# Optimization experiments

Measured on AMD Instinct MI355X. Metric: run time of the kernel, lower is better.

## Reference

```python
import jax, jax.numpy as jnp
import numpy as np

DIM = 384
RED = 16
PAIR = 128
EPS = 1e-5


def setup_inputs() -> dict:
    key = jax.random.key(0)
    ks = jax.random.split(key, 6)
    b, m = 2, 512
    x = jax.random.normal(ks[0], (b, m, DIM), dtype=jnp.float32)
    ln_gamma = jnp.ones((DIM,), dtype=jnp.float32)
    ln_beta = jnp.zeros((DIM,), dtype=jnp.float32)
    w_red = jax.random.normal(ks[1], (DIM, RED), dtype=jnp.float32) / np.sqrt(DIM)
    b_red = jax.random.normal(ks[2], (RED,), dtype=jnp.float32) * 0.02
    w_out = jax.random.normal(ks[3], (RED * RED, PAIR), dtype=jnp.float32) / np.sqrt(RED * RED)
    b_out = jax.random.normal(ks[4], (PAIR,), dtype=jnp.float32) * 0.02
    return {"x": x, "ln_gamma": ln_gamma, "ln_beta": ln_beta,
            "w_red": w_red, "b_red": b_red, "w_out": w_out, "b_out": b_out}


def reference(x, ln_gamma, ln_beta, w_red, b_red, w_out, b_out):
    # LayerNorm over last dim (eps=1e-5, torch default)
    mu = jnp.mean(x, axis=-1, keepdims=True)
    var = jnp.mean(jnp.square(x - mu), axis=-1, keepdims=True)
    xn = (x - mu) * jax.lax.rsqrt(var + EPS) * ln_gamma + ln_beta
    # Linear dim -> 16
    xr = jnp.einsum('bmd,dr->bmr', xn, w_red) + b_red  # (b, m, 16)
    # Full pairwise outer product + projection: same math as
    # einsum('bmi,bnj->bmnij') -> reshape (i j) -> Linear(256, pair_dim),
    # fused so the (i,j) axes contract directly with w_out reshaped to (16,16,pair).
    wr = w_out.reshape(RED, RED, PAIR)
    out = jnp.einsum('bmi,bnj,ijp->bmnp', xr, xr, wr) + b_out  # (b, m, m, pair)
    return out
```

## Files before the change

kernel.cpp:

```cpp
#include <hip/hip_runtime.h>
#include <hip/hip_bf16.h>

#define DIM 384
#define RED 16
#define PAIR 128
#define B 2
#define M 512
#define EPSV 1e-5f
#define LSTR 133

typedef float f32x4 __attribute__((ext_vector_type(4)));
typedef short bf16x8 __attribute__((ext_vector_type(8)));

__device__ __forceinline__ unsigned short f2bf(float f) {
  union { float f; unsigned u; } v; v.f = f;
  unsigned r = v.u + 0x7fffu + ((v.u >> 16) & 1u);
  return (unsigned short)(r >> 16);
}

__global__ __launch_bounds__(128) void opm_k1(
    const float* __restrict__ x, const float* __restrict__ g,
    const float* __restrict__ be, const float* __restrict__ w_red,
    const float* __restrict__ b_red, const float* __restrict__ w_out,
    unsigned short* __restrict__ xr_bf, unsigned short* __restrict__ T_bf) {
  const int row0 = blockIdx.x * 2;
  const int tid  = threadIdx.x;
  const int wave = tid >> 6;
  const int lane = tid & 63;

  __shared__ float xn_s[2][DIM];
  __shared__ float xr_s[2][RED];
  __shared__ float psum[2][4][RED];

  {
    const int row = row0 + wave;
    const float* xrow = x + (size_t)row * DIM;
    float v[6];
    #pragma unroll
    for (int k = 0; k < 6; ++k) v[k] = xrow[lane + 64 * k];
    float s = 0.f, sq = 0.f;
    #pragma unroll
    for (int k = 0; k < 6; ++k) { s += v[k]; sq += v[k] * v[k]; }
    #pragma unroll
    for (int off = 32; off > 0; off >>= 1) {
      s  += __shfl_xor(s, off);
      sq += __shfl_xor(sq, off);
    }
    const float mean = s * (1.0f / DIM);
    const float var  = sq * (1.0f / DIM) - mean * mean;
    const float rstd = rsqrtf(var + EPSV);
    #pragma unroll
    for (int k = 0; k < 6; ++k) {
      const int d = lane + 64 * k;
      xn_s[wave][d] = (v[k] - mean) * rstd * g[d] + be[d];
    }
  }
  __syncthreads();

  {
    const int rw = wave, r = lane & 15, part = lane >> 4;
    const int d0 = part * 96;
    float ps = 0.f;
    #pragma unroll 4
    for (int d = d0; d < d0 + 96; ++d) ps += xn_s[rw][d] * w_red[d * RED + r];
    psum[rw][part][r] = ps;
  }
  __syncthreads();
  if (tid < 32) {
    const int rw = tid >> 4, r = tid & 15;
    float v = b_red[r];
    #pragma unroll
    for (int qq = 0; qq < 4; ++qq) v += psum[rw][qq][r];
    xr_s[rw][r] = v;
    xr_bf[(size_t)(row0 + rw) * RED + r] = f2bf(v);
  }
  __syncthreads();

  {
    const int p = tid;
    const float* W = w_out + p;
    float a0[RED], a1[RED];
    #pragma unroll
    for (int i = 0; i < RED; ++i) {
      float s0 = 0.f, s1 = 0.f;
      #pragma unroll
      for (int j = 0; j < RED; ++j) {
        const float w = W[(i * RED + j) * PAIR];
        s0 += xr_s[0][j] * w;
        s1 += xr_s[1][j] * w;
      }
      a0[i] = s0; a1[i] = s1;
    }
    unsigned int* dst0 = (unsigned int*)(T_bf + ((size_t)row0 * PAIR + p) * RED);
    unsigned int* dst1 = (unsigned int*)(T_bf + ((size_t)(row0 + 1) * PAIR + p) * RED);
    #pragma unroll
    for (int k = 0; k < 8; ++k) {
      dst0[k] = (unsigned)f2bf(a0[2*k]) | ((unsigned)f2bf(a0[2*k+1]) << 16);
      dst1[k] = (unsigned)f2bf(a1[2*k]) | ((unsigned)f2bf(a1[2*k+1]) << 16);
    }
  }
}

__global__ __launch_bounds__(256) void opm_k2(
    const unsigned short* __restrict__ xr_bf, const unsigned short* __restrict__ T_bf,
    const float* __restrict__ b_out, float* __restrict__ out) {
  const int nb = blockIdx.x & 127;
  const int mt = (blockIdx.x >> 7) & 7;
  const int b  = blockIdx.x >> 10;
  const int tid  = threadIdx.x;
  const int wave = tid >> 6;
  const int lane = tid & 63;
  const int q = lane >> 4;
  const int r = lane & 15;
  const int n = nb * 4 + wave;

  __shared__ float lds[64 * LSTR];

  bf16x8 bv[8];
  const unsigned short* Tb = T_bf + ((size_t)(b * M + n) * PAIR) * RED;
  #pragma unroll
  for (int pb = 0; pb < 8; ++pb) {
    bf16x8 v = {0, 0, 0, 0, 0, 0, 0, 0};
    if (q < 2) v = *(const bf16x8*)(Tb + (pb * 16 + r) * RED + q * 8);
    bv[pb] = v;
  }
  float bias[8];
  #pragma unroll
  for (int pb = 0; pb < 8; ++pb) bias[pb] = b_out[pb * 16 + r];

  const int inner  = tid & 127;
  const int n_loc  = inner >> 5;
  const int p4     = (inner & 31) * 4;
  const int mlb    = tid >> 7;

  #pragma unroll
  for (int ms = 0; ms < 4; ++ms) {
    const int m0 = mt * 64 + ms * 16;
    bf16x8 av = {0, 0, 0, 0, 0, 0, 0, 0};
    if (q < 2) av = *(const bf16x8*)(xr_bf + (size_t)(b * M + m0 + r) * RED + q * 8);

    #pragma unroll
    for (int pb = 0; pb < 8; ++pb) {
      f32x4 acc = {bias[pb], bias[pb], bias[pb], bias[pb]};
      acc = __builtin_amdgcn_mfma_f32_16x16x32_bf16(av, bv[pb], acc, 0, 0, 0);
      float* dst = &lds[(wave * 16 + q * 4) * LSTR + pb * 16 + r];
      dst[0]        = acc[0];
      dst[LSTR]     = acc[1];
      dst[2 * LSTR] = acc[2];
      dst[3 * LSTR] = acc[3];
    }
    __syncthreads();

    float* ob = out + ((size_t)(b * M + m0 + mlb) * M + (nb * 4 + n_loc)) * PAIR + p4;
    #pragma unroll
    for (int ps = 0; ps < 8; ++ps) {
      const int m_loc = mlb + ps * 2;
      const f32x4 v = *(const f32x4*)&lds[(n_loc * 16 + m_loc) * LSTR + p4];
      *(f32x4*)(ob + (size_t)ps * 2 * M * PAIR) = v;
    }
    __syncthreads();
  }
}

extern "C" void kernel_launch(void* const* d_in, const int* in_sizes, int n_in,
                              void* d_out, int out_size, void* d_ws, size_t ws_size,
                              hipStream_t stream) {
  const float* x       = (const float*)d_in[0];
  const float* ln_g    = (const float*)d_in[1];
  const float* ln_b    = (const float*)d_in[2];
  const float* w_red   = (const float*)d_in[3];
  const float* b_red   = (const float*)d_in[4];
  const float* w_out   = (const float*)d_in[5];
  const float* b_out   = (const float*)d_in[6];
  float* out = (float*)d_out;

  unsigned short* xr_bf = (unsigned short*)d_ws;
  unsigned short* T_bf  = xr_bf + (size_t)B * M * RED;

  opm_k1<<<B * M / 2, 128, 0, stream>>>(x, ln_g, ln_b, w_red, b_red, w_out, xr_bf, T_bf);
  opm_k2<<<B * (M / 64) * (M / 4), 256, 0, stream>>>(xr_bf, T_bf, b_out, out);
}
```

Before: 61.85 us.

## Use 32x32x16 MFMA with direct nontemporal stores, dropping LDS staging

The second kernel switches from 16x16x32 MFMA with half-zero padded K to 32x32x16 MFMA, which matches K=16 exactly. It also drops the LDS transpose buffer and its two barriers per m-step, writing accumulator registers straight to global memory with nontemporal stores. This removes wasted MFMA work, LDS traffic and synchronisation. The cost is that each store is a scalar 4-byte write; a wave's 32 consecutive lanes still cover 128 contiguous bytes, but the stores are no longer 16-byte vectors.

```diff
diff --git a/kernel.cpp b/kernel.cpp
--- a/kernel.cpp
+++ b/kernel.cpp
@@ -7,9 +7,9 @@
 #define B 2
 #define M 512
 #define EPSV 1e-5f
-#define LSTR 133
 
 typedef float f32x4 __attribute__((ext_vector_type(4)));
+typedef float f32x16 __attribute__((ext_vector_type(16)));
 typedef short bf16x8 __attribute__((ext_vector_type(8)));
 
 __device__ __forceinline__ unsigned short f2bf(float f) {
@@ -107,58 +107,42 @@
   const int nb = blockIdx.x & 127;
   const int mt = (blockIdx.x >> 7) & 7;
   const int b  = blockIdx.x >> 10;
-  const int tid  = threadIdx.x;
-  const int wave = tid >> 6;
-  const int lane = tid & 63;
-  const int q = lane >> 4;
-  const int r = lane & 15;
+  const int wave = threadIdx.x >> 6;
+  const int lane = threadIdx.x & 63;
+  const int c = lane & 31;
+  const int h = lane >> 5;
   const int n = nb * 4 + wave;
 
-  __shared__ float lds[64 * LSTR];
-
-  bf16x8 bv[8];
+  bf16x8 bv[4];
   const unsigned short* Tb = T_bf + ((size_t)(b * M + n) * PAIR) * RED;
   #pragma unroll
-  for (int pb = 0; pb < 8; ++pb) {
-    bf16x8 v = {0, 0, 0, 0, 0, 0, 0, 0};
-    if (q < 2) v = *(const bf16x8*)(Tb + (pb * 16 + r) * RED + q * 8);
-    bv[pb] = v;
-  }
-  float bias[8];
+  for (int pb = 0; pb < 4; ++pb)
+    bv[pb] = *(const bf16x8*)(Tb + (pb * 32 + c) * RED + h * 8);
+
+  float bias[4];
   #pragma unroll
-  for (int pb = 0; pb < 8; ++pb) bias[pb] = b_out[pb * 16 + r];
+  for (int pb = 0; pb < 4; ++pb) bias[pb] = b_out[pb * 32 + c];
 
-  const int inner  = tid & 127;
-  const int n_loc  = inner >> 5;
-  const int p4     = (inner & 31) * 4;
-  const int mlb    = tid >> 7;
+  const size_t MROW = (size_t)M * PAIR;
 
   #pragma unroll
-  for (int ms = 0; ms < 4; ++ms) {
-    const int m0 = mt * 64 + ms * 16;
-    bf16x8 av = {0, 0, 0, 0, 0, 0, 0, 0};
-    if (q < 2) av = *(const bf16x8*)(xr_bf + (size_t)(b * M + m0 + r) * RED + q * 8);
+  for (int ms = 0; ms < 2; ++ms) {
+    const int m0 = mt * 64 + ms * 32;
+    const bf16x8 av = *(const bf16x8*)(xr_bf + (size_t)(b * M + m0 + c) * RED + h * 8);
 
     #pragma unroll
-    for (int pb = 0; pb < 8; ++pb) {
-      f32x4 acc = {bias[pb], bias[pb], bias[pb], bias[pb]};
-      acc = __builtin_amdgcn_mfma_f32_16x16x32_bf16(av, bv[pb], acc, 0, 0, 0);
-      float* dst = &lds[(wave * 16 + q * 4) * LSTR + pb * 16 + r];
-      dst[0]        = acc[0];
-      dst[LSTR]     = acc[1];
-      dst[2 * LSTR] = acc[2];
-      dst[3 * LSTR] = acc[3];
+    for (int pb = 0; pb < 4; ++pb) {
+      f32x16 acc;
+      #pragma unroll
+      for (int k = 0; k < 16; ++k) acc[k] = bias[pb];
+      acc = __builtin_amdgcn_mfma_f32_32x32x16_bf16(av, bv[pb], acc, 0, 0, 0);
+      float* ob = out + ((size_t)(b * M + m0 + h * 4) * M + n) * PAIR + pb * 32 + c;
+      #pragma unroll
+      for (int reg = 0; reg < 16; ++reg) {
+        const int mrow = (reg & 3) + 8 * (reg >> 2);
+        __builtin_nontemporal_store(acc[reg], ob + (size_t)mrow * MROW);
+      }
     }
-    __syncthreads();
-
-    float* ob = out + ((size_t)(b * M + m0 + mlb) * M + (nb * 4 + n_loc)) * PAIR + p4;
-    #pragma unroll
-    for (int ps = 0; ps < 8; ++ps) {
-      const int m_loc = mlb + ps * 2;
-      const f32x4 v = *(const f32x4*)&lds[(n_loc * 16 + m_loc) * LSTR + p4];
-      *(f32x4*)(ob + (size_t)ps * 2 * M * PAIR) = v;
-    }
-    __syncthreads();
   }
 }
 
```

Measured after the change: 67.14 us. 8.6% more time.
